# Performance work log

Hardware: AMD Instinct MI355X
Metric: run time of the kernel (lower is better)

Reference implementation:

```python
import jax, jax.numpy as jnp
import numpy as np
from jax import lax


def _unfold(x, k, s):
    # torch.nn.functional.unfold: [B,C,H,W] -> [B, C*k*k, L], channel-major, row-major kernel offsets
    B, C, H, W = x.shape
    Ho = (H - k) // s + 1
    Wo = (W - k) // s + 1
    patches = [x[:, :, i:i + s * Ho:s, j:j + s * Wo:s] for i in range(k) for j in range(k)]
    stacked = jnp.stack(patches, axis=2)  # [B, C, k*k, Ho, Wo]
    return stacked.reshape(B, C * k * k, Ho * Wo)


def setup_inputs() -> dict:
    key = jax.random.key(0)
    x = jax.random.normal(key, (32, 69, 128, 128), dtype=jnp.float32)
    return {"x": x, "k": 2, "stride": 2}


def reference(x, k, stride):
    B, C, H, W = x.shape
    cs = C - 5  # number of pooled 'shape' channels
    # max pool over the first C-5 channels (kernel k, stride, no padding)
    pooled = lax.reduce_window(x[:, :cs], -jnp.inf, lax.max,
                               (1, 1, k, k), (1, 1, stride, stride), 'VALID')
    Ho, Wo = pooled.shape[2], pooled.shape[3]
    L = Ho * Wo
    kk = k * k
    # per-pixel L1 norm over channels, scaled
    shape_weights = jnp.sum(jnp.abs(x), axis=1, keepdims=True) / np.float32(np.sqrt(cs))
    sw = _unfold(shape_weights, k, stride)  # [B, kk, L]
    query = (sw / jnp.sum(jnp.abs(sw), axis=1, keepdims=True))[:, None]  # [B,1,kk,L]
    u_mean = _unfold(x[:, cs:cs + 2], k, stride).reshape(B, 2, kk, L)
    means = jnp.sum(u_mean * query, axis=2)  # [B,2,L]
    var1 = jnp.sum(_unfold(x[:, cs + 2:cs + 4], k, stride).reshape(B, 2, kk, L) * query, axis=2)
    var2 = jnp.sum((u_mean - means[:, :, None, :]) ** 2 * query, axis=2)
    window_var = var1 + var2
    cov1 = jnp.sum(_unfold(x[:, cs + 4:cs + 5], k, stride).reshape(B, 1, kk, L) * query, axis=2)
    cov2 = jnp.sum((u_mean[:, 0:1] - means[:, 0:1, None, :])
                   * (u_mean[:, 1:2] - means[:, 1:2, None, :])
                   * query ** 2, axis=2)
    window_covar = cov1 + cov2
    # cat + fold with (1,1) kernel == reshape to [B,5,Ho,Wo]
    agg = jnp.concatenate([means, window_var, window_covar], axis=1).reshape(B, 5, Ho, Wo)
    return jnp.concatenate([pooled, agg], axis=1)
```

## Files before the change

kernel.cpp:

```cpp
#include <hip/hip_runtime.h>

#define B_ 32
#define C_ 69
#define CS_ 64
#define H_ 128
#define W_ 128
#define HO_ 64
#define WO_ 64
#define HW_ (H_ * W_)
#define OHW_ (HO_ * WO_)

__global__ __launch_bounds__(256, 8) void spatial_pool_kernel(
        const float* __restrict__ x, float* __restrict__ out) {
    __shared__ float part[4][4][64];
    __shared__ float tail[5][4][64];

    const int lane = threadIdx.x & 63;
    const int w    = threadIdx.x >> 6;
    const int blk  = blockIdx.x;
    const int ho   = blk & 63;
    const int b    = blk >> 6;

    const float* xb = x   + (size_t)b * (C_ * HW_);
    float*       ob = out + (size_t)b * (C_ * OHW_);

    const int base0 = (2 * ho) * W_ + 2 * lane;
    const int base1 = base0 + W_;
    const int opix  = ho * WO_ + lane;

    float S0 = 0.f, S1 = 0.f, S2 = 0.f, S3 = 0.f;

    const int cbeg = w * 17;
    const int cend_pooled = (w == 3) ? CS_ : (cbeg + 17);

    #pragma unroll 4
    for (int c = cbeg; c < cend_pooled; ++c) {
        const float* xc = xb + c * HW_;
        float2 r0 = *(const float2*)(xc + base0);
        float2 r1 = *(const float2*)(xc + base1);
        S0 += fabsf(r0.x); S1 += fabsf(r0.y);
        S2 += fabsf(r1.x); S3 += fabsf(r1.y);
        float m = fmaxf(fmaxf(r0.x, r0.y), fmaxf(r1.x, r1.y));
        ob[c * OHW_ + opix] = m;
    }

    if (w == 3) {
        #pragma unroll
        for (int d = 0; d < 5; ++d) {
            const float* xc = xb + (CS_ + d) * HW_;
            float2 r0 = *(const float2*)(xc + base0);
            float2 r1 = *(const float2*)(xc + base1);
            tail[d][0][lane] = r0.x; tail[d][1][lane] = r0.y;
            tail[d][2][lane] = r1.x; tail[d][3][lane] = r1.y;
            S0 += fabsf(r0.x); S1 += fabsf(r0.y);
            S2 += fabsf(r1.x); S3 += fabsf(r1.y);
        }
    }

    part[w][0][lane] = S0; part[w][1][lane] = S1;
    part[w][2][lane] = S2; part[w][3][lane] = S3;
    __syncthreads();

    if (w == 0) {
        float q[4];
        float tot = 0.f;
        #pragma unroll
        for (int j = 0; j < 4; ++j) {
            q[j] = part[0][j][lane] + part[1][j][lane]
                 + part[2][j][lane] + part[3][j][lane];
            tot += q[j];
        }
        float inv = 1.0f / tot;
        #pragma unroll
        for (int j = 0; j < 4; ++j) q[j] *= inv;

        float sp0[4], sp1[4], sp2[4], sp3[4], sp4[4];
        #pragma unroll
        for (int j = 0; j < 4; ++j) {
            sp0[j] = tail[0][j][lane];
            sp1[j] = tail[1][j][lane];
            sp2[j] = tail[2][j][lane];
            sp3[j] = tail[3][j][lane];
            sp4[j] = tail[4][j][lane];
        }

        float m0 = 0.f, m1 = 0.f;
        #pragma unroll
        for (int j = 0; j < 4; ++j) {
            m0 += sp0[j] * q[j];
            m1 += sp1[j] * q[j];
        }

        float v0 = 0.f, v1 = 0.f, cv = 0.f;
        #pragma unroll
        for (int j = 0; j < 4; ++j) {
            float d0 = sp0[j] - m0;
            float d1 = sp1[j] - m1;
            v0 += sp2[j] * q[j] + d0 * d0 * q[j];
            v1 += sp3[j] * q[j] + d1 * d1 * q[j];
            cv += sp4[j] * q[j] + d0 * d1 * q[j] * q[j];
        }

        ob[(CS_ + 0) * OHW_ + opix] = m0;
        ob[(CS_ + 1) * OHW_ + opix] = m1;
        ob[(CS_ + 2) * OHW_ + opix] = v0;
        ob[(CS_ + 3) * OHW_ + opix] = v1;
        ob[(CS_ + 4) * OHW_ + opix] = cv;
    }
}

extern "C" void kernel_launch(void* const* d_in, const int* in_sizes, int n_in,
                              void* d_out, int out_size, void* d_ws, size_t ws_size,
                              hipStream_t stream) {
    const float* x = (const float*)d_in[0];
    float* out = (float*)d_out;
    const int grid = B_ * HO_;
    spatial_pool_kernel<<<grid, 256, 0, stream>>>(x, out);
}
```

Baseline: 215.3 us.

## Give each thread full channel range and two output pixels, drop shared reduction

Each thread now processes two adjacent output pixels across all channels, using float4 loads and float2 stores. This removes the cross-warp shared-memory reduction and the barrier. Each block now covers 8 output rows instead of one, so the grid is 8x smaller. The cost is much less parallelism and a long serial channel loop per thread, which may hurt latency hiding.

```diff
diff --git a/kernel.cpp b/kernel.cpp
--- a/kernel.cpp
+++ b/kernel.cpp
@@ -10,103 +10,103 @@
 #define HW_ (H_ * W_)
 #define OHW_ (HO_ * WO_)
 
-__global__ __launch_bounds__(256, 8) void spatial_pool_kernel(
+__global__ __launch_bounds__(256) void spatial_pool_kernel(
         const float* __restrict__ x, float* __restrict__ out) {
-    __shared__ float part[4][4][64];
-    __shared__ float tail[5][4][64];
-
     const int lane = threadIdx.x & 63;
     const int w    = threadIdx.x >> 6;
+    const int p    = lane & 31;
+    const int rsel = lane >> 5;
     const int blk  = blockIdx.x;
-    const int ho   = blk & 63;
-    const int b    = blk >> 6;
+    const int b    = blk >> 3;
+    const int ho   = (blk & 7) * 8 + w * 2 + rsel;
 
     const float* xb = x   + (size_t)b * (C_ * HW_);
     float*       ob = out + (size_t)b * (C_ * OHW_);
 
-    const int base0 = (2 * ho) * W_ + 2 * lane;
+    const int base0 = (2 * ho) * W_ + 4 * p;
     const int base1 = base0 + W_;
-    const int opix  = ho * WO_ + lane;
+    const int opix  = ho * WO_ + 2 * p;
 
-    float S0 = 0.f, S1 = 0.f, S2 = 0.f, S3 = 0.f;
-
-    const int cbeg = w * 17;
-    const int cend_pooled = (w == 3) ? CS_ : (cbeg + 17);
+    float Sa0 = 0.f, Sa1 = 0.f, Sa2 = 0.f, Sa3 = 0.f;
+    float Sb0 = 0.f, Sb1 = 0.f, Sb2 = 0.f, Sb3 = 0.f;
 
     #pragma unroll 4
-    for (int c = cbeg; c < cend_pooled; ++c) {
+    for (int c = 0; c < CS_; ++c) {
         const float* xc = xb + c * HW_;
-        float2 r0 = *(const float2*)(xc + base0);
-        float2 r1 = *(const float2*)(xc + base1);
-        S0 += fabsf(r0.x); S1 += fabsf(r0.y);
-        S2 += fabsf(r1.x); S3 += fabsf(r1.y);
-        float m = fmaxf(fmaxf(r0.x, r0.y), fmaxf(r1.x, r1.y));
-        ob[c * OHW_ + opix] = m;
+        float4 r0 = *(const float4*)(xc + base0);
+        float4 r1 = *(const float4*)(xc + base1);
+        Sa0 += fabsf(r0.x); Sa1 += fabsf(r0.y);
+        Sa2 += fabsf(r1.x); Sa3 += fabsf(r1.y);
+        Sb0 += fabsf(r0.z); Sb1 += fabsf(r0.w);
+        Sb2 += fabsf(r1.z); Sb3 += fabsf(r1.w);
+        float2 m;
+        m.x = fmaxf(fmaxf(r0.x, r0.y), fmaxf(r1.x, r1.y));
+        m.y = fmaxf(fmaxf(r0.z, r0.w), fmaxf(r1.z, r1.w));
+        *(float2*)(ob + c * OHW_ + opix) = m;
     }
 
-    if (w == 3) {
-        #pragma unroll
-        for (int d = 0; d < 5; ++d) {
-            const float* xc = xb + (CS_ + d) * HW_;
-            float2 r0 = *(const float2*)(xc + base0);
-            float2 r1 = *(const float2*)(xc + base1);
-            tail[d][0][lane] = r0.x; tail[d][1][lane] = r0.y;
-            tail[d][2][lane] = r1.x; tail[d][3][lane] = r1.y;
-            S0 += fabsf(r0.x); S1 += fabsf(r0.y);
-            S2 += fabsf(r1.x); S3 += fabsf(r1.y);
-        }
+    float4 t0[5], t1[5];
+    #pragma unroll
+    for (int d = 0; d < 5; ++d) {
+        const float* xc = xb + (CS_ + d) * HW_;
+        t0[d] = *(const float4*)(xc + base0);
+        t1[d] = *(const float4*)(xc + base1);
+        Sa0 += fabsf(t0[d].x); Sa1 += fabsf(t0[d].y);
+        Sa2 += fabsf(t1[d].x); Sa3 += fabsf(t1[d].y);
+        Sb0 += fabsf(t0[d].z); Sb1 += fabsf(t0[d].w);
+        Sb2 += fabsf(t1[d].z); Sb3 += fabsf(t1[d].w);
     }
 
-    part[w][0][lane] = S0; part[w][1][lane] = S1;
-    part[w][2][lane] = S2; part[w][3][lane] = S3;
-    __syncthreads();
-
-    if (w == 0) {
-        float q[4];
-        float tot = 0.f;
-        #pragma unroll
-        for (int j = 0; j < 4; ++j) {
-            q[j] = part[0][j][lane] + part[1][j][lane]
-                 + part[2][j][lane] + part[3][j][lane];
-            tot += q[j];
+    float2 res[5];
+    #pragma unroll
+    for (int pix = 0; pix < 2; ++pix) {
+        float q0, q1, q2, q3;
+        float v64[4], v65[4], v66[4], v67[4], v68[4];
+        if (pix == 0) {
+            q0 = Sa0; q1 = Sa1; q2 = Sa2; q3 = Sa3;
+            #pragma unroll
+            for (int d = 0; d < 1; ++d) {}
+            v64[0] = t0[0].x; v64[1] = t0[0].y; v64[2] = t1[0].x; v64[3] = t1[0].y;
+            v65[0] = t0[1].x; v65[1] = t0[1].y; v65[2] = t1[1].x; v65[3] = t1[1].y;
+            v66[0] = t0[2].x; v66[1] = t0[2].y; v66[2] = t1[2].x; v66[3] = t1[2].y;
+            v67[0] = t0[3].x; v67[1] = t0[3].y; v67[2] = t1[3].x; v67[3] = t1[3].y;
+            v68[0] = t0[4].x; v68[1] = t0[4].y; v68[2] = t1[4].x; v68[3] = t1[4].y;
+        } else {
+            q0 = Sb0; q1 = Sb1; q2 = Sb2; q3 = Sb3;
+            v64[0] = t0[0].z; v64[1] = t0[0].w; v64[2] = t1[0].z; v64[3] = t1[0].w;
+            v65[0] = t0[1].z; v65[1] = t0[1].w; v65[2] = t1[1].z; v65[3] = t1[1].w;
+            v66[0] = t0[2].z; v66[1] = t0[2].w; v66[2] = t1[2].z; v66[3] = t1[2].w;
+            v67[0] = t0[3].z; v67[1] = t0[3].w; v67[2] = t1[3].z; v67[3] = t1[3].w;
+            v68[0] = t0[4].z; v68[1] = t0[4].w; v68[2] = t1[4].z; v68[3] = t1[4].w;
         }
-        float inv = 1.0f / tot;
-        #pragma unroll
-        for (int j = 0; j < 4; ++j) q[j] *= inv;
-
-        float sp0[4], sp1[4], sp2[4], sp3[4], sp4[4];
-        #pragma unroll
-        for (int j = 0; j < 4; ++j) {
-            sp0[j] = tail[0][j][lane];
-            sp1[j] = tail[1][j][lane];
-            sp2[j] = tail[2][j][lane];
-            sp3[j] = tail[3][j][lane];
-            sp4[j] = tail[4][j][lane];
-        }
+        float inv = 1.0f / (q0 + q1 + q2 + q3);
+        float q[4] = {q0 * inv, q1 * inv, q2 * inv, q3 * inv};
 
         float m0 = 0.f, m1 = 0.f;
         #pragma unroll
         for (int j = 0; j < 4; ++j) {
-            m0 += sp0[j] * q[j];
-            m1 += sp1[j] * q[j];
+            m0 += v64[j] * q[j];
+            m1 += v65[j] * q[j];
         }
-
-        float v0 = 0.f, v1 = 0.f, cv = 0.f;
+        float vv0 = 0.f, vv1 = 0.f, cv = 0.f;
         #pragma unroll
         for (int j = 0; j < 4; ++j) {
-            float d0 = sp0[j] - m0;
-            float d1 = sp1[j] - m1;
-            v0 += sp2[j] * q[j] + d0 * d0 * q[j];
-            v1 += sp3[j] * q[j] + d1 * d1 * q[j];
-            cv += sp4[j] * q[j] + d0 * d1 * q[j] * q[j];
+            float d0 = v64[j] - m0;
+            float d1 = v65[j] - m1;
+            vv0 += v66[j] * q[j] + d0 * d0 * q[j];
+            vv1 += v67[j] * q[j] + d1 * d1 * q[j];
+            cv  += v68[j] * q[j] + d0 * d1 * q[j] * q[j];
         }
+        if (pix == 0) {
+            res[0].x = m0; res[1].x = m1; res[2].x = vv0; res[3].x = vv1; res[4].x = cv;
+        } else {
+            res[0].y = m0; res[1].y = m1; res[2].y = vv0; res[3].y = vv1; res[4].y = cv;
+        }
+    }
 
-        ob[(CS_ + 0) * OHW_ + opix] = m0;
-        ob[(CS_ + 1) * OHW_ + opix] = m1;
-        ob[(CS_ + 2) * OHW_ + opix] = v0;
-        ob[(CS_ + 3) * OHW_ + opix] = v1;
-        ob[(CS_ + 4) * OHW_ + opix] = cv;
-    }
+    #pragma unroll
+    for (int d = 0; d < 5; ++d)
+        *(float2*)(ob + (CS_ + d) * OHW_ + opix) = res[d];
 }
 
 extern "C" void kernel_launch(void* const* d_in, const int* in_sizes, int n_in,
@@ -114,6 +114,6 @@
                               hipStream_t stream) {
     const float* x = (const float*)d_in[0];
     float* out = (float*)d_out;
-    const int grid = B_ * HO_;
+    const int grid = B_ * (HO_ / 8);
     spatial_pool_kernel<<<grid, 256, 0, stream>>>(x, out);
 }
```

New measurement: 214.8 us. No clear change (-0.2%).
